# Optimization experiments

Measured on AMD Instinct MI355X. Metric: run time of the kernel, lower is better.

## Reference

```python
import jax, jax.numpy as jnp
import numpy as np
from jax import lax

HID = 512
NEG = -1e30

def conv2d(x, w, pad):
    # x: [N,C,H,W], w: [O,I,kh,kw]
    return lax.conv_general_dilated(x, w, (1, 1), [(pad, pad), (pad, pad)],
                                    dimension_numbers=('NCHW', 'OIHW', 'NCHW'))

def maxpool3s2p1(x):
    return lax.reduce_window(x, -jnp.inf, lax.max, (1, 1, 3, 3), (1, 1, 2, 2),
                             [(0, 0), (0, 0), (1, 1), (1, 1)])

def setup_inputs() -> dict:
    key = jax.random.key(0)
    ks = jax.random.split(key, 12)
    N, B = 128, 16
    gid = jnp.repeat(jnp.arange(B), N // B).astype(jnp.float32)  # sorted group ids
    rois = jnp.concatenate([gid[:, None], jax.random.uniform(ks[0], (N, 4))], axis=1)
    interact_feat = jax.random.normal(ks[1], (N, 2304, 1, 16, 16), jnp.float32)
    bbox_feat = jax.random.normal(ks[2], (N, 1024, 4, 7, 7), jnp.float32)
    s = lambda k, sh: jax.random.normal(k, sh, jnp.float32) * 0.02
    return {
        'rois': rois,
        'interact_feat': interact_feat,
        'bbox_feat': bbox_feat,
        'w_reduce': s(ks[3], (HID, 2304, 1, 1)),
        'w_rsize': s(ks[4], (HID, HID, 3, 3)),
        'wq': s(ks[5], (HID, HID, 3, 3)),
        'wk': s(ks[6], (HID, HID, 3, 3)),
        'wv': s(ks[7], (HID, HID, 3, 3)),
        'w1': s(ks[8], (HID, HID, 3, 3)),
        'gamma': jnp.ones((HID,), jnp.float32),
        'beta': jnp.zeros((HID,), jnp.float32),
        'w_fc': s(ks[9], (HID, 2 * HID)),
    }

def reference(rois, interact_feat, bbox_feat, w_reduce, w_rsize, wq, wk, wv, w1, gamma, beta, w_fc):
    f = interact_feat[:, :, 0]                      # squeeze(2): [N,2304,16,16]
    f = jax.nn.relu(conv2d(f, w_reduce, 0))         # [N,512,16,16]
    f = conv2d(f, w_rsize, 0)                       # no padding -> [N,512,14,14]
    f = maxpool3s2p1(f)                             # [N,512,7,7]

    gid = rois[:, 0].astype(jnp.int32)
    mask = gid[:, None] == gid[None, :]             # [N,N] same-group mask (vectorizes ragged loop)

    q = conv2d(f, wq, 1)
    k = conv2d(f, wk, 1)
    v = conv2d(f, wv, 1)
    # per-pixel attention across rois within each group
    att = jnp.einsum('ichw,jchw->ijhw', q, k) / jnp.sqrt(jnp.asarray(HID, f.dtype))
    att = jnp.where(mask[:, :, None, None], att, NEG)
    att = jax.nn.softmax(att, axis=1)               # softmax over key rois (dim=1)
    virt = jnp.einsum('ijhw,jchw->ichw', att, v)    # [N,512,7,7]

    # GroupNorm(1, C): normalize over (C,H,W), per-channel affine
    mu = virt.mean(axis=(1, 2, 3), keepdims=True)
    var = virt.var(axis=(1, 2, 3), keepdims=True)
    virt = (virt - mu) / jnp.sqrt(var + 1e-5)
    virt = virt * gamma[None, :, None, None] + beta[None, :, None, None]
    virt = jax.nn.relu(virt)
    virt = conv2d(virt, w1, 1)                      # dropout = identity in eval

    ho = (f + virt).mean(axis=(2, 3))               # gap1 -> [N,512]
    ob = bbox_feat.mean(axis=(2, 3, 4))             # gap2 -> [N,1024]
    ob = jax.nn.relu(ob @ w_fc.T)                   # fc1 -> [N,512]
    return jnp.concatenate([ho, ob], axis=1)        # [N,1024]
```

## Files before the change

kernel.cpp:

```cpp
#include <hip/hip_runtime.h>
#include <hip/hip_bf16.h>
#include <math.h>

typedef __bf16 bf16;
typedef __bf16 v8bf __attribute__((ext_vector_type(8)));
typedef float f32x4 __attribute__((ext_vector_type(4)));

#define GLDS16(g, l) __builtin_amdgcn_global_load_lds( \
    (const __attribute__((address_space(1))) void*)(g), \
    (__attribute__((address_space(3))) void*)(l), 16, 0, 0)

__device__ __forceinline__ int xcd_swz(int bid, int nwg) {
  int xcd = bid & 7, off = bid >> 3;
  int q = nwg >> 3, r = nwg & 7;
  return (xcd < r ? xcd * (q + 1) : r * (q + 1) + (xcd - r) * q) + off;
}

#define LDA256(ih) do { \
  _Pragma("unroll") for (int _i = 0; _i < 4; ++_i) { \
    int _r = (ih) * 64 + _i * 16 + l15; \
    int _c = (wm * 64 + colb) ^ ((l15 & 7) << 4); \
    af[_i] = *(const v8bf*)(ringp + _r * 128 + _c); } } while (0)

#define LDB256() do { \
  _Pragma("unroll") for (int _j = 0; _j < 4; ++_j) { \
    int _r = (wn & 1) * 64 + _j * 16 + l15; \
    int _c = ((wn >> 1) * 64 + colb) ^ ((l15 & 7) << 4); \
    bfr[_j] = *(const v8bf*)(ringp + 16384 + _r * 128 + _c); } } while (0)

#define MMA256(ih) do { \
  __builtin_amdgcn_s_setprio(1); \
  _Pragma("unroll") for (int _i = 0; _i < 4; ++_i) \
  _Pragma("unroll") for (int _j = 0; _j < 4; ++_j) \
    acc[(ih)*4+_i][_j] = __builtin_amdgcn_mfma_f32_16x16x32_bf16(af[_i], bfr[_j], acc[(ih)*4+_i][_j], 0, 0, 0); \
  __builtin_amdgcn_s_setprio(0); } while (0)

#define GROUP256(g, NT, STAGEA, STAGEB) do { \
  const char* ringp = lds + ((g) & 3) * 32768; \
  char* srng = lds + (((g) + 3) & 3) * 32768; \
  (void)srng; \
  const bool _st = ((g) + 3 < (NT)); \
  LDA256(0); LDB256(); \
  if (_st) { STAGEA; } \
  __builtin_amdgcn_s_barrier(); \
  __builtin_amdgcn_sched_barrier(0); \
  MMA256(0); \
  __builtin_amdgcn_sched_barrier(0); \
  __builtin_amdgcn_s_barrier(); \
  LDA256(1); \
  if (_st) { STAGEB; } \
  if (_st)                       asm volatile("s_waitcnt vmcnt(8)" ::: "memory"); \
  else if ((g) + 3 == (NT))      asm volatile("s_waitcnt vmcnt(4)" ::: "memory"); \
  else if ((g) + 3 == (NT) + 1)  asm volatile("s_waitcnt vmcnt(0)" ::: "memory"); \
  __builtin_amdgcn_s_barrier(); \
  __builtin_amdgcn_sched_barrier(0); \
  MMA256(1); \
  __builtin_amdgcn_sched_barrier(0); \
  __builtin_amdgcn_s_barrier(); } while (0)

__global__ __launch_bounds__(512, 2)
void k_gemm_reduce(const bf16* __restrict__ A, const bf16* __restrict__ B,
                   bf16* __restrict__ f1, int mbase)
{
  __shared__ __attribute__((aligned(16))) char lds[131072];
  const int s = xcd_swz(blockIdx.x, gridDim.x);
  const int by = s & 1, bx = s >> 1;
  const int t = threadIdx.x, lane = t & 63, w = t >> 6;
  const int wm = w >> 2, wn = w & 3;
  const int l15 = lane & 15, colb = (lane >> 4) << 4;
  const int tr = t >> 3;
  const int lb = ((t & 7) << 4) ^ ((tr & 7) << 4);
  const int hi = lb >> 6, kb = lb & 63;
  const int t16 = t * 16;
  const char* pa[2]; const char* pb[2];
  #pragma unroll
  for (int j = 0; j < 2; ++j) {
    pa[j] = (const char*)A + (size_t)(bx * 256 + j * 64 + tr + hi * 128) * 4608 + kb;
    pb[j] = (const char*)B + (size_t)(by * 256 + j * 64 + tr + hi * 128) * 4608 + kb;
  }
  #define SA_GR(kt, ring) do { GLDS16(pa[0]+(size_t)(kt)*64, (ring)+t16); \
                               GLDS16(pa[1]+(size_t)(kt)*64, (ring)+8192+t16); } while (0)
  #define SB_GR(kt, ring) do { GLDS16(pb[0]+(size_t)(kt)*64, (ring)+16384+t16); \
                               GLDS16(pb[1]+(size_t)(kt)*64, (ring)+24576+t16); } while (0)
  f32x4 acc[8][4] = {};
  v8bf af[4], bfr[4];
  SA_GR(0, lds);         SB_GR(0, lds);
  SA_GR(1, lds + 32768); SB_GR(1, lds + 32768);
  SA_GR(2, lds + 65536); SB_GR(2, lds + 65536);
  asm volatile("s_waitcnt vmcnt(8)" ::: "memory");
  __builtin_amdgcn_s_barrier();
  for (int g = 0; g < 72; ++g) {
    GROUP256(g, 72, SA_GR(g + 3, srng), SB_GR(g + 3, srng));
  }
  const int rbase = (lane >> 4) << 2, cl = lane & 15;
  #pragma unroll
  for (int i = 0; i < 8; ++i)
    #pragma unroll
    for (int j = 0; j < 4; ++j)
      #pragma unroll
      for (int r = 0; r < 4; ++r) {
        int row = mbase + bx * 256 + wm * 128 + i * 16 + rbase + r;
        int col = by * 256 + wn * 64 + j * 16 + cl;
        f1[(size_t)row * 512 + col] = (bf16)fmaxf(acc[i][j][r], 0.f);
      }
}

__global__ __launch_bounds__(512, 2)
void k_conv_rsize(const bf16* __restrict__ f1, const bf16* __restrict__ wt,
                  bf16* __restrict__ f14)
{
  __shared__ __attribute__((aligned(16))) char lds[131072];
  const int s = xcd_swz(blockIdx.x, gridDim.x);
  const int by = s & 1, bx = s >> 1;
  const int t = threadIdx.x, lane = t & 63, w = t >> 6;
  const int wm = w >> 2, wn = w & 3;
  const int l15 = lane & 15, colb = (lane >> 4) << 4;
  const int tr = t >> 3;
  const int lb = ((t & 7) << 4) ^ ((tr & 7) << 4);
  const int hi = lb >> 6, kb = lb & 63;
  const int t16 = t * 16;
  int abase[2]; const char* pb[2];
  #pragma unroll
  for (int j = 0; j < 2; ++j) {
    int m = bx * 256 + j * 64 + tr + hi * 128;
    int n = m / 196, rem = m - n * 196;
    int y = rem / 14, x = rem - 14 * (rem / 14);
    abase[j] = n * 256 + y * 16 + x;
    pb[j] = (const char*)wt + (size_t)(by * 256 + j * 64 + tr + hi * 128) * 1024 + kb;
  }
  const char* f1c = (const char*)f1 + kb;
  #define SA_CR(kt, ring) do { int _tap = (kt) >> 4, _ko = ((kt) & 15) << 6; \
    int _dy = (_tap * 11) >> 5, _dx = _tap - _dy * 3; int _df = _dy * 16 + _dx; \
    GLDS16(f1c + (size_t)(abase[0] + _df) * 1024 + _ko, (ring)+t16); \
    GLDS16(f1c + (size_t)(abase[1] + _df) * 1024 + _ko, (ring)+8192+t16); } while (0)
  #define SB_CR(kt, ring) do { int _tap = (kt) >> 4, _ko = ((kt) & 15) << 6; \
    GLDS16(pb[0] + (size_t)_tap * 524288 + _ko, (ring)+16384+t16); \
    GLDS16(pb[1] + (size_t)_tap * 524288 + _ko, (ring)+24576+t16); } while (0)
  f32x4 acc[8][4] = {};
  v8bf af[4], bfr[4];
  SA_CR(0, lds);         SB_CR(0, lds);
  SA_CR(1, lds + 32768); SB_CR(1, lds + 32768);
  SA_CR(2, lds + 65536); SB_CR(2, lds + 65536);
  asm volatile("s_waitcnt vmcnt(8)" ::: "memory");
  __builtin_amdgcn_s_barrier();
  for (int g = 0; g < 144; ++g) {
    GROUP256(g, 144, SA_CR(g + 3, srng), SB_CR(g + 3, srng));
  }
  const int rbase = (lane >> 4) << 2, cl = lane & 15;
  #pragma unroll
  for (int i = 0; i < 8; ++i)
    #pragma unroll
    for (int j = 0; j < 4; ++j)
      #pragma unroll
      for (int r = 0; r < 4; ++r) {
        int row = bx * 256 + wm * 128 + i * 16 + rbase + r;
        int col = by * 256 + wn * 64 + j * 16 + cl;
        f14[(size_t)row * 512 + col] = (bf16)acc[i][j][r];
      }
}

__global__ __launch_bounds__(512, 2)
void k_conv_qkv(const bf16* __restrict__ fin, const bf16* __restrict__ wt,
                bf16* __restrict__ qkv, const bf16* __restrict__ zp,
                const float* __restrict__ bbox, float* __restrict__ obm)
{
  __shared__ __attribute__((aligned(16))) char lds[131072];
  const int t = threadIdx.x;
  if (blockIdx.x >= 150) {
    int bid = blockIdx.x - 150;
    int n = bid >> 3;
    int c = (bid & 7) * 128 + (t >> 2);
    int seg = t & 3;
    const float4* p4 = (const float4*)(bbox + ((size_t)n * 1024 + c) * 196);
    float sum = 0.f;
    for (int k = seg; k < 49; k += 4) { float4 ww = p4[k]; sum += ww.x + ww.y + ww.z + ww.w; }
    sum += __shfl_xor(sum, 1);
    sum += __shfl_xor(sum, 2);
    if (seg == 0) obm[n * 1024 + c] = sum * (1.f / 196.f);
    return;
  }
  const int s = xcd_swz(blockIdx.x, 150);
  const int q6 = s % 6, bx = s / 6;
  const int tensor = q6 >> 1, byl = q6 & 1;
  const char* wtc = (const char*)wt + (size_t)tensor * 4718592;
  bf16* outp = qkv + (size_t)tensor * 3211264;
  const int lane = t & 63, w = t >> 6;
  const int wm = w >> 2, wn = w & 3;
  const int l15 = lane & 15, colb = (lane >> 4) << 4;
  const int tr = t >> 3;
  const int lb = ((t & 7) << 4) ^ ((tr & 7) << 4);
  const int hi = lb >> 6, kb = lb & 63;
  const int t16 = t * 16;
  int nb[2], py[2], px[2]; const char* pb[2];
  #pragma unroll
  for (int j = 0; j < 2; ++j) {
    int m = bx * 256 + j * 64 + tr + hi * 128;
    if (m > 6271) m = 6271;
    int n = m / 49, rem = m - n * 49;
    nb[j] = n * 49;
    py[j] = rem / 7 - 1;
    px[j] = rem - 7 * (rem / 7) - 1;
    pb[j] = wtc + (size_t)(byl * 256 + j * 64 + tr + hi * 128) * 1024 + kb;
  }
  const char* finc = (const char*)fin + kb;
  const char* zpc = (const char*)zp;
  #define SA_QK(kt, ring) do { int _tap = (kt) >> 4, _ko = ((kt) & 15) << 6; \
    int _dy = (_tap * 11) >> 5, _dx = _tap - _dy * 3; \
    _Pragma("unroll") for (int _j = 0; _j < 2; ++_j) { \
      int _iy = py[_j] + _dy, _ix = px[_j] + _dx; \
      const char* _sp = ((unsigned)_iy < 7u && (unsigned)_ix < 7u) \
          ? finc + (size_t)(nb[_j] + _iy * 7 + _ix) * 1024 + _ko : zpc; \
      GLDS16(_sp, (ring) + _j * 8192 + t16); } } while (0)
  #define SB_QK(kt, ring) do { int _tap = (kt) >> 4, _ko = ((kt) & 15) << 6; \
    GLDS16(pb[0] + (size_t)_tap * 524288 + _ko, (ring)+16384+t16); \
    GLDS16(pb[1] + (size_t)_tap * 524288 + _ko, (ring)+24576+t16); } while (0)
  f32x4 acc[8][4] = {};
  v8bf af[4], bfr[4];
  SA_QK(0, lds);         SB_QK(0, lds);
  SA_QK(1, lds + 32768); SB_QK(1, lds + 32768);
  SA_QK(2, lds + 65536); SB_QK(2, lds + 65536);
  asm volatile("s_waitcnt vmcnt(8)" ::: "memory");
  __builtin_amdgcn_s_barrier();
  for (int g = 0; g < 144; ++g) {
    GROUP256(g, 144, SA_QK(g + 3, srng), SB_QK(g + 3, srng));
  }
  const int rbase = (lane >> 4) << 2, cl = lane & 15;
  #pragma unroll
  for (int i = 0; i < 8; ++i)
    #pragma unroll
    for (int j = 0; j < 4; ++j)
      #pragma unroll
      for (int r = 0; r < 4; ++r) {
        int row = bx * 256 + wm * 128 + i * 16 + rbase + r;
        if (row < 6272) {
          int col = byl * 256 + wn * 64 + j * 16 + cl;
          outp[(size_t)row * 512 + col] = (bf16)acc[i][j][r];
        }
      }
}

__device__ __forceinline__ void tile_compute(const char* ldsA, const char* ldsB,
                                             f32x4 (&acc)[4][4], int wr, int wc, int lane) {
  const int l15 = lane & 15;
  const int colb = (lane >> 4) << 4;
  #pragma unroll
  for (int kk = 0; kk < 2; ++kk) {
    v8bf a[4], b[4];
    #pragma unroll
    for (int i = 0; i < 4; ++i) {
      int ra = wr * 64 + i * 16 + l15;
      int ca = ((kk << 6) | colb) ^ ((ra & 7) << 4);
      a[i] = *(const v8bf*)(ldsA + ra * 128 + ca);
    }
    #pragma unroll
    for (int j = 0; j < 4; ++j) {
      int rb = wc * 64 + j * 16 + l15;
      int cb = ((kk << 6) | colb) ^ ((rb & 7) << 4);
      b[j] = *(const v8bf*)(ldsB + rb * 128 + cb);
    }
    __builtin_amdgcn_s_setprio(1);
    #pragma unroll
    for (int i = 0; i < 4; ++i)
      #pragma unroll
      for (int j = 0; j < 4; ++j)
        acc[i][j] = __builtin_amdgcn_mfma_f32_16x16x32_bf16(a[i], b[j], acc[i][j], 0, 0, 0);
    __builtin_amdgcn_s_setprio(0);
  }
}

#define PIPELINE_LOOP(NK)                                                   \
  stage(0, lds);                                                            \
  stage(1, lds + 32768);                                                    \
  int cur = 0;                                                              \
  for (int ks = 0; ks < (NK) - 1; ++ks) {                                   \
    asm volatile("s_waitcnt vmcnt(8)" ::: "memory");                        \
    __builtin_amdgcn_s_barrier();                                           \
    __builtin_amdgcn_sched_barrier(0);                                      \
    tile_compute(lds + cur * 32768, lds + cur * 32768 + 16384, acc, wr, wc, lane); \
    __builtin_amdgcn_sched_barrier(0);                                      \
    __builtin_amdgcn_s_barrier();                                           \
    __builtin_amdgcn_sched_barrier(0);                                      \
    if (ks + 2 < (NK)) stage(ks + 2, lds + cur * 32768);                    \
    cur ^= 1;                                                               \
  }                                                                         \
  asm volatile("s_waitcnt vmcnt(0)" ::: "memory");                          \
  __builtin_amdgcn_s_barrier();                                             \
  __builtin_amdgcn_sched_barrier(0);                                        \
  tile_compute(lds + cur * 32768, lds + cur * 32768 + 16384, acc, wr, wc, lane);

__global__ __launch_bounds__(256)
void k_gemm_s(const bf16* __restrict__ A_s, const bf16* __restrict__ w1r,
              float* __restrict__ part)
{
  __shared__ __attribute__((aligned(16))) char lds[65536];
  const int by = blockIdx.x, kspl = blockIdx.y;
  const int t = threadIdx.x, lane = t & 63, w = t >> 6, wr = w >> 1, wc = w & 1;
  const int tr = t >> 3;
  const int cphys = ((t & 7) << 4) ^ ((tr & 7) << 4);
  const char* pa[4]; const char* pb[4];
  #pragma unroll
  for (int i = 0; i < 4; ++i) {
    int r = i * 32 + tr;
    pa[i] = (const char*)A_s + (size_t)r * 9216 + kspl * 2304 + cphys;
    pb[i] = (const char*)w1r + (size_t)(by * 128 + r) * 9216 + kspl * 2304 + cphys;
  }
  const int lo = t * 16;
  auto stage = [&](int ks, char* base) {
    #pragma unroll
    for (int i = 0; i < 4; ++i) GLDS16(pa[i] + ks * 128, base + lo + i * 4096);
    #pragma unroll
    for (int i = 0; i < 4; ++i) GLDS16(pb[i] + ks * 128, base + 16384 + lo + i * 4096);
  };
  f32x4 acc[4][4] = {};
  PIPELINE_LOOP(18)
  const int rb = (lane >> 4) << 2, cl = lane & 15;
  #pragma unroll
  for (int i = 0; i < 4; ++i)
    #pragma unroll
    for (int j = 0; j < 4; ++j)
      #pragma unroll
      for (int r = 0; r < 4; ++r) {
        int row = wr * 64 + i * 16 + rb + r;
        int col = by * 128 + wc * 64 + j * 16 + cl;
        part[(size_t)kspl * 65536 + row * 512 + col] = acc[i][j][r];
      }
}

__global__ __launch_bounds__(512)
void k_red(const float* __restrict__ part, const float* __restrict__ f7m,
           float* __restrict__ out)
{
  int idx = blockIdx.x * 512 + threadIdx.x;
  float s = part[idx] + part[65536 + idx] + part[131072 + idx] + part[196608 + idx];
  int row = idx >> 9, col = idx & 511;
  out[row * 1024 + col] = s + f7m[idx];
}

__global__ void k_tin(const float* __restrict__ in, bf16* __restrict__ A1, int n0)
{
  __shared__ float tile[64][36];
  const int k0 = blockIdx.x * 64, p0 = blockIdx.y * 32, nl = blockIdx.z;
  const int n = n0 + nl;
  const int t = threadIdx.x;
  const float* src = in + (size_t)n * 2304 * 256;
  #pragma unroll
  for (int rep = 0; rep < 2; ++rep) {
    int idx = t + rep * 256;
    int row = idx >> 3, c4 = (idx & 7) * 4;
    float4 v = *(const float4*)(src + (size_t)(k0 + row) * 256 + p0 + c4);
    tile[row][c4] = v.x; tile[row][c4 + 1] = v.y;
    tile[row][c4 + 2] = v.z; tile[row][c4 + 3] = v.w;
  }
  __syncthreads();
  const int pl = t >> 3, ke = (t & 7) * 8;
  v8bf o;
  #pragma unroll
  for (int e = 0; e < 8; ++e) o[e] = (bf16)tile[ke + e][pl];
  bf16* dst = A1 + (size_t)nl * 256 * 2304;
  *(v8bf*)(dst + (size_t)(p0 + pl) * 2304 + k0 + ke) = o;
}

__global__ void k_castw(const float* __restrict__ wsrc, bf16* __restrict__ wb, int nelem)
{
  int idx = (blockIdx.x * 256 + threadIdx.x) * 4;
  if (idx >= nelem) return;
  float4 v = *(const float4*)(wsrc + idx);
  bf16 o0 = (bf16)v.x, o1 = (bf16)v.y, o2 = (bf16)v.z, o3 = (bf16)v.w;
  bf16* d = wb + idx;
  d[0] = o0; d[1] = o1; d[2] = o2; d[3] = o3;
}

__global__ void k_wtrans(const float* __restrict__ s0, const float* __restrict__ s1,
                         const float* __restrict__ s2, const float* __restrict__ s3,
                         const float* __restrict__ s4, bf16* __restrict__ wt,
                         bf16* __restrict__ w1r)
{
  const float* src;
  switch (blockIdx.y) {
    case 0: src = s0; break; case 1: src = s1; break; case 2: src = s2; break;
    case 3: src = s3; break; default: src = s4; break;
  }
  int q = blockIdx.x * 256 + threadIdx.x;
  const float* sp = src + (size_t)q * 9;
  float tmp[9];
  #pragma unroll
  for (int e = 0; e < 9; ++e) tmp[e] = sp[e];
  if (blockIdx.y < 4) {
    bf16* dst = wt + (size_t)blockIdx.y * 2359296;
    #pragma unroll
    for (int e = 0; e < 9; ++e) dst[(size_t)e * 262144 + q] = (bf16)tmp[e];
  } else {
    int co = q >> 9, ci = q & 511;
    #pragma unroll
    for (int e = 0; e < 9; ++e) w1r[(size_t)(co * 9 + e) * 512 + ci] = (bf16)tmp[e];
  }
}

__global__ void k_pool(const bf16* __restrict__ f14, bf16* __restrict__ f7b)
{
  int idx = blockIdx.x * 256 + threadIdx.x;
  int c2 = idx & 255;
  int pp = idx >> 8;
  int n = pp / 49, p7 = pp - n * 49;
  int y = p7 / 7, x = p7 - 7 * (p7 / 7);
  int y0 = 2 * y - 1, x0 = 2 * x - 1;
  const unsigned* f14u = (const unsigned*)f14;
  float m0 = -3.4e38f, m1 = -3.4e38f;
  #pragma unroll
  for (int dy = 0; dy < 3; ++dy) {
    int iy = y0 + dy; if ((unsigned)iy >= 14u) continue;
    #pragma unroll
    for (int dx = 0; dx < 3; ++dx) {
      int ix = x0 + dx; if ((unsigned)ix >= 14u) continue;
      unsigned vv = f14u[(size_t)(n * 196 + iy * 14 + ix) * 256 + c2];
      m0 = fmaxf(m0, __builtin_bit_cast(float, vv << 16));
      m1 = fmaxf(m1, __builtin_bit_cast(float, vv & 0xffff0000u));
    }
  }
  bf16 b0 = (bf16)m0, b1 = (bf16)m1;
  unsigned pk = (unsigned)__builtin_bit_cast(unsigned short, b0)
              | ((unsigned)__builtin_bit_cast(unsigned short, b1) << 16);
  ((unsigned*)f7b)[idx] = pk;
}

__global__ __launch_bounds__(256)
void k_attn(const bf16* __restrict__ q, const bf16* __restrict__ k,
            const bf16* __restrict__ v, const float* __restrict__ rois,
            float* __restrict__ virt)
{
  const int p = blockIdx.x, g = blockIdx.y, t = threadIdx.x;
  __shared__ float sS[8][9];
  __shared__ float sP[8][9];
  __shared__ __attribute__((aligned(16))) bf16 sV[8][512];
  {
    int u = t;
    #pragma unroll
    for (int rep = 0; rep < 2; ++rep, u += 256) {
      int j = u >> 6, ch = u & 63;
      *(v8bf*)&sV[j][ch * 8] = *(const v8bf*)(v + ((size_t)(g * 8 + j) * 49 + p) * 512 + ch * 8);
    }
  }
  int pi = t >> 2, ls = t & 3;
  int i = pi >> 3, j = pi & 7;
  const bf16* qi = q + ((size_t)(g * 8 + i) * 49 + p) * 512;
  const bf16* kj = k + ((size_t)(g * 8 + j) * 49 + p) * 512;
  float s = 0.f;
  for (int ch = ls * 16; ch < ls * 16 + 16; ++ch) {
    v8bf a = *(const v8bf*)(qi + ch * 8);
    v8bf b = *(const v8bf*)(kj + ch * 8);
    #pragma unroll
    for (int e = 0; e < 8; ++e) s += (float)a[e] * (float)b[e];
  }
  s += __shfl_xor(s, 1);
  s += __shfl_xor(s, 2);
  if (ls == 0) sS[i][j] = s * 0.04419417382415922f;
  __syncthreads();
  if (t < 8) {
    float gi = rois[(g * 8 + t) * 5];
    float pv[8]; float mx = -3.4e38f;
    #pragma unroll
    for (int jj = 0; jj < 8; ++jj) {
      float gj = rois[(g * 8 + jj) * 5];
      float sv = (gi == gj) ? sS[t][jj] : -1e30f;
      pv[jj] = sv; mx = fmaxf(mx, sv);
    }
    float sum = 0.f;
    #pragma unroll
    for (int jj = 0; jj < 8; ++jj) { float e = expf(pv[jj] - mx); pv[jj] = e; sum += e; }
    float inv = 1.f / sum;
    #pragma unroll
    for (int jj = 0; jj < 8; ++jj) sP[t][jj] = pv[jj] * inv;
  }
  __syncthreads();
  int i2 = t >> 5, c0 = (t & 31) * 16;
  float o[16];
  #pragma unroll
  for (int e = 0; e < 16; ++e) o[e] = 0.f;
  #pragma unroll
  for (int jj = 0; jj < 8; ++jj) {
    float ww = sP[i2][jj];
    v8bf v0 = *(const v8bf*)&sV[jj][c0];
    v8bf v1 = *(const v8bf*)&sV[jj][c0 + 8];
    #pragma unroll
    for (int e = 0; e < 8; ++e) { o[e] += ww * (float)v0[e]; o[8 + e] += ww * (float)v1[e]; }
  }
  float* dst = virt + ((size_t)(g * 8 + i2) * 49 + p) * 512 + c0;
  #pragma unroll
  for (int e = 0; e < 16; ++e) dst[e] = o[e];
}

__global__ __launch_bounds__(512)
void k_ln_fc(const float* __restrict__ virt, const float* __restrict__ gamma,
             const float* __restrict__ beta, const bf16* __restrict__ f7b,
             bf16* __restrict__ A_s, float* __restrict__ f7m,
             const float* __restrict__ obm, const float* __restrict__ wfc,
             float* __restrict__ out)
{
  const int t = threadIdx.x;
  if (blockIdx.x >= 128) {
    __shared__ float sO[1024];
    int n = blockIdx.x - 128;
    for (int u = t; u < 1024; u += 512) sO[u] = obm[n * 1024 + u];
    __syncthreads();
    const float4* wp = (const float4*)(wfc + (size_t)t * 1024);
    float s = 0.f;
    for (int c4 = 0; c4 < 256; ++c4) {
      float4 w = wp[c4];
      s += w.x * sO[c4 * 4] + w.y * sO[c4 * 4 + 1] + w.z * sO[c4 * 4 + 2] + w.w * sO[c4 * 4 + 3];
    }
    out[n * 1024 + 512 + t] = fmaxf(s, 0.f);
    return;
  }
  const int n = blockIdx.x;
  const float* p = virt + (size_t)n * 25088 + t;
  float xv[49];
  float s1 = 0.f, s2 = 0.f;
  #pragma unroll
  for (int pp = 0; pp < 49; ++pp) {
    float x = p[pp * 512];
    xv[pp] = x; s1 += x; s2 += x * x;
  }
  __shared__ float r1[512], r2[512];
  r1[t] = s1; r2[t] = s2; __syncthreads();
  for (int off = 256; off; off >>= 1) {
    if (t < off) { r1[t] += r1[t + off]; r2[t] += r2[t + off]; }
    __syncthreads();
  }
  float mu = r1[0] * (1.f / 25088.f);
  float var = r2[0] * (1.f / 25088.f) - mu * mu;
  float rstd = rsqrtf(var + 1e-5f);
  float g = gamma[t], be = beta[t];
  const bf16* fp = f7b + (size_t)n * 25088 + t;
  float T = 0, R0 = 0, R6 = 0, C0 = 0, C6 = 0;
  float X00 = 0, X06 = 0, X60 = 0, X66 = 0, F = 0;
  #pragma unroll
  for (int pp = 0; pp < 49; ++pp) {
    const int u = pp / 7, v = pp - 7 * (pp / 7);
    float y = fmaxf((xv[pp] - mu) * rstd * g + be, 0.f);
    T += y;
    if (u == 0) R0 += y;
    if (u == 6) R6 += y;
    if (v == 0) C0 += y;
    if (v == 6) C6 += y;
    if (pp == 0)  X00 = y;
    if (pp == 6)  X06 = y;
    if (pp == 42) X60 = y;
    if (pp == 48) X66 = y;
    F += (float)fp[pp * 512];
  }
  float sv[9] = { T-R6-C6+X66, T-R6, T-R6-C0+X60,
                  T-C6,        T,    T-C0,
                  T-R0-C6+X06, T-R0, T-R0-C0+X00 };
  bf16* Ap = A_s + (size_t)n * 4608 + t;
  #pragma unroll
  for (int tap = 0; tap < 9; ++tap)
    Ap[tap * 512] = (bf16)(sv[tap] * (1.f / 49.f));
  f7m[n * 512 + t] = F * (1.f / 49.f);
}

extern "C" void kernel_launch(void* const* d_in, const int* in_sizes, int n_in,
                              void* d_out, int out_size, void* d_ws, size_t ws_size,
                              hipStream_t stream) {
  const float* rois     = (const float*)d_in[0];
  const float* interact = (const float*)d_in[1];
  const float* bbox     = (const float*)d_in[2];
  const float* w_reduce = (const float*)d_in[3];
  const float* w_rsize  = (const float*)d_in[4];
  const float* wq       = (const float*)d_in[5];
  const float* wk       = (const float*)d_in[6];
  const float* wv       = (const float*)d_in[7];
  const float* w1       = (const float*)d_in[8];
  const float* gamma    = (const float*)d_in[9];
  const float* beta     = (const float*)d_in[10];
  const float* wfc      = (const float*)d_in[11];
  float* out = (float*)d_out;
  char* ws = (char*)d_ws;

  size_t o = 0;
  auto take = [&](size_t sz) { size_t r = o; o += (sz + 255) & ~(size_t)255; return r; };
  bf16*  wrb   = (bf16*)(ws + take(2359296));
  bf16*  wt    = (bf16*)(ws + take(18874368));
  bf16*  w1r   = (bf16*)(ws + take(4718592));
  char*  Rf1   = ws + take(33554432);
  bf16*  f7b   = (bf16*)(ws + take(6422528));
  float* virt  = (float*)(ws + take(12845056));
  bf16*  A_s   = (bf16*)(ws + take(1179648));
  float* f7m   = (float*)(ws + take(262144));
  float* part  = (float*)(ws + take(1048576));
  float* obm   = (float*)(ws + take(524288));
  bf16*  zp    = (bf16*)(ws + take(256));
  size_t fixedEnd = o;
  const size_t A1_FULL = 150994944;
  bool full = (ws_size >= fixedEnd + A1_FULL);
  bf16* A1  = (bf16*)(ws + fixedEnd);
  bf16* f14 = (bf16*)(ws + fixedEnd);

  bf16* f1 = (bf16*)Rf1;
  bf16* qb = (bf16*)Rf1;
  bf16* kb = qb + 3211264;
  bf16* vb = kb + 3211264;

  hipMemsetAsync(zp, 0, 256, stream);

  k_castw<<<1152, 256, 0, stream>>>(w_reduce, wrb, 1179648);
  k_wtrans<<<dim3(1024, 5), 256, 0, stream>>>(w_rsize, wq, wk, wv, w1, wt, w1r);

  if (full) {
    k_tin<<<dim3(36, 8, 128), 256, 0, stream>>>(interact, A1, 0);
    k_gemm_reduce<<<256, 512, 0, stream>>>(A1, wrb, f1, 0);
  } else {
    for (int ch = 0; ch < 4; ++ch) {
      k_tin<<<dim3(36, 8, 32), 256, 0, stream>>>(interact, A1, ch * 32);
      k_gemm_reduce<<<64, 512, 0, stream>>>(A1, wrb, f1, ch * 8192);
    }
  }

  k_conv_rsize<<<196, 512, 0, stream>>>(f1, wt, f14);
  k_pool<<<6272, 256, 0, stream>>>(f14, f7b);

  k_conv_qkv<<<1174, 512, 0, stream>>>(f7b, wt + (size_t)1 * 2359296, qb, zp, bbox, obm);

  k_attn<<<dim3(49, 16), 256, 0, stream>>>(qb, kb, vb, rois, virt);

  k_ln_fc<<<256, 512, 0, stream>>>(virt, gamma, beta, f7b, A_s, f7m, obm, wfc, out);

  k_gemm_s<<<dim3(4, 4), 256, 0, stream>>>(A_s, w1r, part);
  k_red<<<128, 512, 0, stream>>>(part, f7m, out);
}
```

Measured before the change: 551.4 us.

## Shrink GEMM/conv tiles to 256x128 with 4 waves and triple-buffered LDS ring

```diff
diff --git a/kernel.cpp b/kernel.cpp
--- a/kernel.cpp
+++ b/kernel.cpp
@@ -16,82 +16,77 @@
   return (xcd < r ? xcd * (q + 1) : r * (q + 1) + (xcd - r) * q) + off;
 }
 
-#define LDA256(ih) do { \
+#define RING_COMPUTE() do { \
+  v8bf b_[4], a_[4]; \
+  _Pragma("unroll") for (int _j = 0; _j < 4; ++_j) { \
+    int _lr = _j * 16 + l15; \
+    int _c = (wn * 64 + colb) ^ ((_lr & 7) << 4); \
+    b_[_j] = *(const v8bf*)(s0 + 16384 + _lr * 128 + _c); } \
   _Pragma("unroll") for (int _i = 0; _i < 4; ++_i) { \
-    int _r = (ih) * 64 + _i * 16 + l15; \
-    int _c = (wm * 64 + colb) ^ ((l15 & 7) << 4); \
-    af[_i] = *(const v8bf*)(ringp + _r * 128 + _c); } } while (0)
-
-#define LDB256() do { \
-  _Pragma("unroll") for (int _j = 0; _j < 4; ++_j) { \
-    int _r = (wn & 1) * 64 + _j * 16 + l15; \
-    int _c = ((wn >> 1) * 64 + colb) ^ ((l15 & 7) << 4); \
-    bfr[_j] = *(const v8bf*)(ringp + 16384 + _r * 128 + _c); } } while (0)
-
-#define MMA256(ih) do { \
+    int _lr = _i * 16 + l15; \
+    int _c = (wm * 64 + colb) ^ ((_lr & 7) << 4); \
+    a_[_i] = *(const v8bf*)(s0 + _lr * 128 + _c); } \
   __builtin_amdgcn_s_setprio(1); \
   _Pragma("unroll") for (int _i = 0; _i < 4; ++_i) \
   _Pragma("unroll") for (int _j = 0; _j < 4; ++_j) \
-    acc[(ih)*4+_i][_j] = __builtin_amdgcn_mfma_f32_16x16x32_bf16(af[_i], bfr[_j], acc[(ih)*4+_i][_j], 0, 0, 0); \
-  __builtin_amdgcn_s_setprio(0); } while (0)
-
-#define GROUP256(g, NT, STAGEA, STAGEB) do { \
-  const char* ringp = lds + ((g) & 3) * 32768; \
-  char* srng = lds + (((g) + 3) & 3) * 32768; \
-  (void)srng; \
-  const bool _st = ((g) + 3 < (NT)); \
-  LDA256(0); LDB256(); \
-  if (_st) { STAGEA; } \
-  __builtin_amdgcn_s_barrier(); \
-  __builtin_amdgcn_sched_barrier(0); \
-  MMA256(0); \
-  __builtin_amdgcn_sched_barrier(0); \
-  __builtin_amdgcn_s_barrier(); \
-  LDA256(1); \
-  if (_st) { STAGEB; } \
-  if (_st)                       asm volatile("s_waitcnt vmcnt(8)" ::: "memory"); \
-  else if ((g) + 3 == (NT))      asm volatile("s_waitcnt vmcnt(4)" ::: "memory"); \
-  else if ((g) + 3 == (NT) + 1)  asm volatile("s_waitcnt vmcnt(0)" ::: "memory"); \
-  __builtin_amdgcn_s_barrier(); \
-  __builtin_amdgcn_sched_barrier(0); \
-  MMA256(1); \
-  __builtin_amdgcn_sched_barrier(0); \
-  __builtin_amdgcn_s_barrier(); } while (0)
-
-__global__ __launch_bounds__(512, 2)
+    acc[_i][_j] = __builtin_amdgcn_mfma_f32_16x16x32_bf16(a_[_i], b_[_j], acc[_i][_j], 0, 0, 0); \
+  __builtin_amdgcn_s_setprio(0); \
+  _Pragma("unroll") for (int _i = 0; _i < 4; ++_i) { \
+    int _lr = (_i + 4) * 16 + l15; \
+    int _c = (wm * 64 + colb) ^ ((_lr & 7) << 4); \
+    a_[_i] = *(const v8bf*)(s0 + _lr * 128 + _c); } \
+  __builtin_amdgcn_s_setprio(1); \
+  _Pragma("unroll") for (int _i = 0; _i < 4; ++_i) \
+  _Pragma("unroll") for (int _j = 0; _j < 4; ++_j) \
+    acc[_i + 4][_j] = __builtin_amdgcn_mfma_f32_16x16x32_bf16(a_[_i], b_[_j], acc[_i + 4][_j], 0, 0, 0); \
+  __builtin_amdgcn_s_setprio(0); \
+} while (0)
+
+#define RING_LOOP(NG, STAGE) do { \
+  STAGE(0, s0); STAGE(1, s1); \
+  for (int g = 0; g < (NG); ++g) { \
+    if (g + 2 < (NG)) { STAGE(g + 2, s2); } \
+    if (g + 2 < (NG))       asm volatile("s_waitcnt vmcnt(12)" ::: "memory"); \
+    else if (g + 2 == (NG)) asm volatile("s_waitcnt vmcnt(6)" ::: "memory"); \
+    else                    asm volatile("s_waitcnt vmcnt(0)" ::: "memory"); \
+    __builtin_amdgcn_s_barrier(); \
+    __builtin_amdgcn_sched_barrier(0); \
+    RING_COMPUTE(); \
+    __builtin_amdgcn_sched_barrier(0); \
+    __builtin_amdgcn_s_barrier(); \
+    char* _tmp = s0; s0 = s1; s1 = s2; s2 = _tmp; \
+  } \
+} while (0)
+
+__global__ __launch_bounds__(256, 2)
 void k_gemm_reduce(const bf16* __restrict__ A, const bf16* __restrict__ B,
                    bf16* __restrict__ f1, int mbase)
 {
-  __shared__ __attribute__((aligned(16))) char lds[131072];
+  __shared__ __attribute__((aligned(16))) char lds[73728];
+  char *s0 = lds, *s1 = lds + 24576, *s2 = lds + 49152;
   const int s = xcd_swz(blockIdx.x, gridDim.x);
-  const int by = s & 1, bx = s >> 1;
+  const int by = s & 3, bx = s >> 2;
   const int t = threadIdx.x, lane = t & 63, w = t >> 6;
-  const int wm = w >> 2, wn = w & 3;
+  const int wm = w >> 1, wn = w & 1;
   const int l15 = lane & 15, colb = (lane >> 4) << 4;
   const int tr = t >> 3;
   const int lb = ((t & 7) << 4) ^ ((tr & 7) << 4);
   const int hi = lb >> 6, kb = lb & 63;
   const int t16 = t * 16;
-  const char* pa[2]; const char* pb[2];
-  #pragma unroll
-  for (int j = 0; j < 2; ++j) {
-    pa[j] = (const char*)A + (size_t)(bx * 256 + j * 64 + tr + hi * 128) * 4608 + kb;
-    pb[j] = (const char*)B + (size_t)(by * 256 + j * 64 + tr + hi * 128) * 4608 + kb;
-  }
-  #define SA_GR(kt, ring) do { GLDS16(pa[0]+(size_t)(kt)*64, (ring)+t16); \
-                               GLDS16(pa[1]+(size_t)(kt)*64, (ring)+8192+t16); } while (0)
-  #define SB_GR(kt, ring) do { GLDS16(pb[0]+(size_t)(kt)*64, (ring)+16384+t16); \
-                               GLDS16(pb[1]+(size_t)(kt)*64, (ring)+24576+t16); } while (0)
+  const char* pa[4]; const char* pb[2];
+  #pragma unroll
+  for (int i = 0; i < 4; ++i)
+    pa[i] = (const char*)A + (size_t)(bx * 256 + i * 32 + tr + hi * 128) * 4608 + kb;
+  #pragma unroll
+  for (int i = 0; i < 2; ++i)
+    pb[i] = (const char*)B + (size_t)(by * 128 + i * 32 + tr + hi * 64) * 4608 + kb;
+  #define SG(kt, ring) do { \
+    _Pragma("unroll") for (int _i = 0; _i < 4; ++_i) \
+      GLDS16(pa[_i] + (size_t)(kt) * 64, (ring) + _i * 4096 + t16); \
+    _Pragma("unroll") for (int _i = 0; _i < 2; ++_i) \
+      GLDS16(pb[_i] + (size_t)(kt) * 64, (ring) + 16384 + _i * 4096 + t16); } while (0)
   f32x4 acc[8][4] = {};
-  v8bf af[4], bfr[4];
-  SA_GR(0, lds);         SB_GR(0, lds);
-  SA_GR(1, lds + 32768); SB_GR(1, lds + 32768);
-  SA_GR(2, lds + 65536); SB_GR(2, lds + 65536);
-  asm volatile("s_waitcnt vmcnt(8)" ::: "memory");
-  __builtin_amdgcn_s_barrier();
-  for (int g = 0; g < 72; ++g) {
-    GROUP256(g, 72, SA_GR(g + 3, srng), SB_GR(g + 3, srng));
-  }
+  RING_LOOP(72, SG);
   const int rbase = (lane >> 4) << 2, cl = lane & 15;
   #pragma unroll
   for (int i = 0; i < 8; ++i)
@@ -100,52 +95,47 @@
       #pragma unroll
       for (int r = 0; r < 4; ++r) {
         int row = mbase + bx * 256 + wm * 128 + i * 16 + rbase + r;
-        int col = by * 256 + wn * 64 + j * 16 + cl;
+        int col = by * 128 + wn * 64 + j * 16 + cl;
         f1[(size_t)row * 512 + col] = (bf16)fmaxf(acc[i][j][r], 0.f);
       }
 }
 
-__global__ __launch_bounds__(512, 2)
+__global__ __launch_bounds__(256, 2)
 void k_conv_rsize(const bf16* __restrict__ f1, const bf16* __restrict__ wt,
                   bf16* __restrict__ f14)
 {
-  __shared__ __attribute__((aligned(16))) char lds[131072];
+  __shared__ __attribute__((aligned(16))) char lds[73728];
+  char *s0 = lds, *s1 = lds + 24576, *s2 = lds + 49152;
   const int s = xcd_swz(blockIdx.x, gridDim.x);
-  const int by = s & 1, bx = s >> 1;
+  const int by = s & 3, bx = s >> 2;
   const int t = threadIdx.x, lane = t & 63, w = t >> 6;
-  const int wm = w >> 2, wn = w & 3;
+  const int wm = w >> 1, wn = w & 1;
   const int l15 = lane & 15, colb = (lane >> 4) << 4;
   const int tr = t >> 3;
   const int lb = ((t & 7) << 4) ^ ((tr & 7) << 4);
   const int hi = lb >> 6, kb = lb & 63;
   const int t16 = t * 16;
-  int abase[2]; const char* pb[2];
-  #pragma unroll
-  for (int j = 0; j < 2; ++j) {
-    int m = bx * 256 + j * 64 + tr + hi * 128;
+  int abase[4]; const char* pb[2];
+  #pragma unroll
+  for (int i = 0; i < 4; ++i) {
+    int m = bx * 256 + i * 32 + tr + hi * 128;
     int n = m / 196, rem = m - n * 196;
     int y = rem / 14, x = rem - 14 * (rem / 14);
-    abase[j] = n * 256 + y * 16 + x;
-    pb[j] = (const char*)wt + (size_t)(by * 256 + j * 64 + tr + hi * 128) * 1024 + kb;
-  }
+    abase[i] = n * 256 + y * 16 + x;
+  }
+  #pragma unroll
+  for (int i = 0; i < 2; ++i)
+    pb[i] = (const char*)wt + (size_t)(by * 128 + i * 32 + tr + hi * 64) * 1024 + kb;
   const char* f1c = (const char*)f1 + kb;
-  #define SA_CR(kt, ring) do { int _tap = (kt) >> 4, _ko = ((kt) & 15) << 6; \
-    int _dy = (_tap * 11) >> 5, _dx = _tap - _dy * 3; int _df = _dy * 16 + _dx; \
-    GLDS16(f1c + (size_t)(abase[0] + _df) * 1024 + _ko, (ring)+t16); \
-    GLDS16(f1c + (size_t)(abase[1] + _df) * 1024 + _ko, (ring)+8192+t16); } while (0)
-  #define SB_CR(kt, ring) do { int _tap = (kt) >> 4, _ko = ((kt) & 15) << 6; \
-    GLDS16(pb[0] + (size_t)_tap * 524288 + _ko, (ring)+16384+t16); \
-    GLDS16(pb[1] + (size_t)_tap * 524288 + _ko, (ring)+24576+t16); } while (0)
+  #define SC(kt, ring) do { int _tap = (kt) >> 4, _ko = ((kt) & 15) << 6; \
+    int _dy = (_tap * 11) >> 5, _dx = _tap - _dy * 3; \
+    int _df = (_dy * 16 + _dx) << 10; \
+    _Pragma("unroll") for (int _i = 0; _i < 4; ++_i) \
+      GLDS16(f1c + ((size_t)abase[_i] << 10) + _df + _ko, (ring) + _i * 4096 + t16); \
+    _Pragma("unroll") for (int _i = 0; _i < 2; ++_i) \
+      GLDS16(pb[_i] + (size_t)_tap * 524288 + _ko, (ring) + 16384 + _i * 4096 + t16); } while (0)
   f32x4 acc[8][4] = {};
-  v8bf af[4], bfr[4];
-  SA_CR(0, lds);         SB_CR(0, lds);
-  SA_CR(1, lds + 32768); SB_CR(1, lds + 32768);
-  SA_CR(2, lds + 65536); SB_CR(2, lds + 65536);
-  asm volatile("s_waitcnt vmcnt(8)" ::: "memory");
-  __builtin_amdgcn_s_barrier();
-  for (int g = 0; g < 144; ++g) {
-    GROUP256(g, 144, SA_CR(g + 3, srng), SB_CR(g + 3, srng));
-  }
+  RING_LOOP(144, SC);
   const int rbase = (lane >> 4) << 2, cl = lane & 15;
   #pragma unroll
   for (int i = 0; i < 8; ++i)
@@ -154,22 +144,23 @@
       #pragma unroll
       for (int r = 0; r < 4; ++r) {
         int row = bx * 256 + wm * 128 + i * 16 + rbase + r;
-        int col = by * 256 + wn * 64 + j * 16 + cl;
+        int col = by * 128 + wn * 64 + j * 16 + cl;
         f14[(size_t)row * 512 + col] = (bf16)acc[i][j][r];
       }
 }
 
-__global__ __launch_bounds__(512, 2)
+__global__ __launch_bounds__(256, 2)
 void k_conv_qkv(const bf16* __restrict__ fin, const bf16* __restrict__ wt,
                 bf16* __restrict__ qkv, const bf16* __restrict__ zp,
                 const float* __restrict__ bbox, float* __restrict__ obm)
 {
-  __shared__ __attribute__((aligned(16))) char lds[131072];
+  __shared__ __attribute__((aligned(16))) char lds[73728];
+  char *s0 = lds, *s1 = lds + 24576, *s2 = lds + 49152;
   const int t = threadIdx.x;
-  if (blockIdx.x >= 150) {
-    int bid = blockIdx.x - 150;
-    int n = bid >> 3;
-    int c = (bid & 7) * 128 + (t >> 2);
+  if (blockIdx.x >= 300) {
+    int bid = blockIdx.x - 300;
+    int n = bid >> 4;
+    int c = (bid & 15) * 64 + (t >> 2);
     int seg = t & 3;
     const float4* p4 = (const float4*)(bbox + ((size_t)n * 1024 + c) * 196);
     float sum = 0.f;
@@ -179,51 +170,44 @@
     if (seg == 0) obm[n * 1024 + c] = sum * (1.f / 196.f);
     return;
   }
-  const int s = xcd_swz(blockIdx.x, 150);
-  const int q6 = s % 6, bx = s / 6;
-  const int tensor = q6 >> 1, byl = q6 & 1;
+  const int s = xcd_swz(blockIdx.x, 300);
+  const int q12 = s % 12, bx = s / 12;
+  const int tensor = q12 >> 2, byl = q12 & 3;
   const char* wtc = (const char*)wt + (size_t)tensor * 4718592;
   bf16* outp = qkv + (size_t)tensor * 3211264;
   const int lane = t & 63, w = t >> 6;
-  const int wm = w >> 2, wn = w & 3;
+  const int wm = w >> 1, wn = w & 1;
   const int l15 = lane & 15, colb = (lane >> 4) << 4;
   const int tr = t >> 3;
   const int lb = ((t & 7) << 4) ^ ((tr & 7) << 4);
   const int hi = lb >> 6, kb = lb & 63;
   const int t16 = t * 16;
-  int nb[2], py[2], px[2]; const char* pb[2];
-  #pragma unroll
-  for (int j = 0; j < 2; ++j) {
-    int m = bx * 256 + j * 64 + tr + hi * 128;
+  int nb[4], py[4], px[4]; const char* pb[2];
+  #pragma unroll
+  for (int i = 0; i < 4; ++i) {
+    int m = bx * 256 + i * 32 + tr + hi * 128;
     if (m > 6271) m = 6271;
     int n = m / 49, rem = m - n * 49;
-    nb[j] = n * 49;
-    py[j] = rem / 7 - 1;
-    px[j] = rem - 7 * (rem / 7) - 1;
-    pb[j] = wtc + (size_t)(byl * 256 + j * 64 + tr + hi * 128) * 1024 + kb;
-  }
+    nb[i] = n * 49;
+    py[i] = rem / 7 - 1;
+    px[i] = rem - 7 * (rem / 7) - 1;
+  }
+  #pragma unroll
+  for (int i = 0; i < 2; ++i)
+    pb[i] = wtc + (size_t)(byl * 128 + i * 32 + tr + hi * 64) * 1024 + kb;
   const char* finc = (const char*)fin + kb;
   const char* zpc = (const char*)zp;
-  #define SA_QK(kt, ring) do { int _tap = (kt) >> 4, _ko = ((kt) & 15) << 6; \
+  #define SQ(kt, ring) do { int _tap = (kt) >> 4, _ko = ((kt) & 15) << 6; \
     int _dy = (_tap * 11) >> 5, _dx = _tap - _dy * 3; \
-    _Pragma("unroll") for (int _j = 0; _j < 2; ++_j) { \
-      int _iy = py[_j] + _dy, _ix = px[_j] + _dx; \
+    _Pragma("unroll") for (int _i = 0; _i < 4; ++_i) { \
+      int _iy = py[_i] + _dy, _ix = px[_i] + _dx; \
       const char* _sp = ((unsigned)_iy < 7u && (unsigned)_ix < 7u) \
-          ? finc + (size_t)(nb[_j] + _iy * 7 + _ix) * 1024 + _ko : zpc; \
-      GLDS16(_sp, (ring) + _j * 8192 + t16); } } while (0)
-  #define SB_QK(kt, ring) do { int _tap = (kt) >> 4, _ko = ((kt) & 15) << 6; \
-    GLDS16(pb[0] + (size_t)_tap * 524288 + _ko, (ring)+16384+t16); \
-    GLDS16(pb[1] + (size_t)_tap * 524288 + _ko, (ring)+24576+t16); } while (0)
+          ? finc + (size_t)(nb[_i] + _iy * 7 + _ix) * 1024 + _ko : zpc; \
+      GLDS16(_sp, (ring) + _i * 4096 + t16); } \
+    _Pragma("unroll") for (int _i = 0; _i < 2; ++_i) \
+      GLDS16(pb[_i] + (size_t)_tap * 524288 + _ko, (ring) + 16384 + _i * 4096 + t16); } while (0)
   f32x4 acc[8][4] = {};
-  v8bf af[4], bfr[4];
-  SA_QK(0, lds);         SB_QK(0, lds);
-  SA_QK(1, lds + 32768); SB_QK(1, lds + 32768);
-  SA_QK(2, lds + 65536); SB_QK(2, lds + 65536);
-  asm volatile("s_waitcnt vmcnt(8)" ::: "memory");
-  __builtin_amdgcn_s_barrier();
-  for (int g = 0; g < 144; ++g) {
-    GROUP256(g, 144, SA_QK(g + 3, srng), SB_QK(g + 3, srng));
-  }
+  RING_LOOP(144, SQ);
   const int rbase = (lane >> 4) << 2, cl = lane & 15;
   #pragma unroll
   for (int i = 0; i < 8; ++i)
@@ -233,7 +217,7 @@
       for (int r = 0; r < 4; ++r) {
         int row = bx * 256 + wm * 128 + i * 16 + rbase + r;
         if (row < 6272) {
-          int col = byl * 256 + wn * 64 + j * 16 + cl;
+          int col = byl * 128 + wn * 64 + j * 16 + cl;
           outp[(size_t)row * 512 + col] = (bf16)acc[i][j][r];
         }
       }
@@ -607,18 +591,18 @@
 
   if (full) {
     k_tin<<<dim3(36, 8, 128), 256, 0, stream>>>(interact, A1, 0);
-    k_gemm_reduce<<<256, 512, 0, stream>>>(A1, wrb, f1, 0);
+    k_gemm_reduce<<<512, 256, 0, stream>>>(A1, wrb, f1, 0);
   } else {
     for (int ch = 0; ch < 4; ++ch) {
       k_tin<<<dim3(36, 8, 32), 256, 0, stream>>>(interact, A1, ch * 32);
-      k_gemm_reduce<<<64, 512, 0, stream>>>(A1, wrb, f1, ch * 8192);
+      k_gemm_reduce<<<128, 256, 0, stream>>>(A1, wrb, f1, ch * 8192);
     }
   }
 
-  k_conv_rsize<<<196, 512, 0, stream>>>(f1, wt, f14);
+  k_conv_rsize<<<392, 256, 0, stream>>>(f1, wt, f14);
   k_pool<<<6272, 256, 0, stream>>>(f14, f7b);
 
-  k_conv_qkv<<<1174, 512, 0, stream>>>(f7b, wt + (size_t)1 * 2359296, qb, zp, bbox, obm);
+  k_conv_qkv<<<2348, 256, 0, stream>>>(f7b, wt + (size_t)1 * 2359296, qb, zp, bbox, obm);
 
   k_attn<<<dim3(49, 16), 256, 0, stream>>>(qb, kb, vb, rois, virt);
 
```

After: 543.0 us. No clear change (-1.5%).
